# Optimization experiments

Measured on AMD Instinct MI355X. Metric: run time of the kernel, lower is better.

The kernel has to match this reference:

```python
import jax, jax.numpy as jnp
import numpy as np

N_TOKENS = 8192
D_MODEL = 1024
HD_DIM = 4096
N_VEC = 32
N_EXP = 12


def setup_inputs() -> dict:
    key = jax.random.key(0)
    k1, k2, k3, k4, k5 = jax.random.split(key, 5)
    # Glorot-style scaling for the bases so activations stay O(1)
    s_up = (2.0 / (D_MODEL + HD_DIM)) ** 0.5
    return {
        "inputs": jax.random.normal(k1, (N_TOKENS, D_MODEL), dtype=jnp.float32),
        "shared_basis_up": jax.random.normal(k2, (N_VEC, D_MODEL, HD_DIM), dtype=jnp.float32) * s_up,
        "shared_basis_down": jax.random.normal(k3, (N_VEC, HD_DIM, D_MODEL), dtype=jnp.float32) * s_up,
        "expert_coeffs_up": jax.random.normal(k4, (N_EXP, N_VEC), dtype=jnp.float32) * 0.5,
        "expert_coeffs_down": jax.random.normal(k5, (N_EXP, N_VEC), dtype=jnp.float32) * 0.5,
        "expert_bias": jnp.zeros((N_EXP, D_MODEL), dtype=jnp.float32),
        "expert_idx": 3,
    }


def reference(inputs, shared_basis_up, shared_basis_down, expert_coeffs_up,
              expert_coeffs_down, expert_bias, expert_idx):
    coeffs_up = expert_coeffs_up[expert_idx]      # [v]
    coeffs_down = expert_coeffs_down[expert_idx]  # [v]
    bias = expert_bias[expert_idx]                # [d_model]
    # Reconstruct expert weights from shared basis
    W_up = jnp.einsum('v,vdh->dh', coeffs_up, shared_basis_up)      # [d_model, hd_dim]
    W_down = jnp.einsum('v,vhd->hd', coeffs_down, shared_basis_down)  # [hd_dim, d_model]
    hidden = jax.nn.gelu(inputs @ W_up, approximate=False)  # TF default gelu is exact (erf)
    return hidden @ W_down + bias
```

## Files before the change

kernel.cpp:

```cpp
#include <hip/hip_runtime.h>
#include <cstdint>

#define NTOK 8192
#define DMODEL 1024
#define HDDIM 4096
#define NVEC 32

typedef float f32x4_v __attribute__((ext_vector_type(4)));
typedef __bf16 bf16x8 __attribute__((ext_vector_type(8)));
typedef unsigned short u16x4 __attribute__((ext_vector_type(4)));
typedef unsigned short u16x8 __attribute__((ext_vector_type(8)));

__device__ __forceinline__ unsigned short f2bf(float f) {
  union { float f; uint32_t u; } x; x.f = f;
  uint32_t r = (x.u + 0x7FFFu + ((x.u >> 16) & 1u)) >> 16;
  return (unsigned short)r;
}

__device__ __forceinline__ float gelu_fast(float x) {
  float t = x * x;
  float z = x * (2.3022082f + 0.1029440f * t);
  float e = exp2f(-z);
  return x / (1.0f + e);
}

#define VMCNT(n) asm volatile("s_waitcnt vmcnt(" #n ")" ::: "memory")

__device__ __forceinline__ void gload16(const unsigned short* g, unsigned short* lds)
{
  __builtin_amdgcn_global_load_lds((__attribute__((address_space(1))) void*)g,
                                   (__attribute__((address_space(3))) void*)lds,
                                   16, 0, 0);
}

__device__ __forceinline__
void reconstruct_body(const float* __restrict__ basis,
                      const float* __restrict__ coeffs,
                      int e, unsigned short* __restrict__ outT,
                      int X, int Y, int tile, int stag, char* smem, int t)
{
  float (*lds)[260] = (float (*)[260])smem;
  const int xtiles = X >> 4;
  const int bx = tile % xtiles;
  const int by = tile / xtiles;
  const int x0 = bx << 4, y0 = by << 8;
  const int w  = t >> 6, l = t & 63;

  f32x4_v acc[4];
  #pragma unroll
  for (int i = 0; i < 4; ++i) acc[i] = (f32x4_v){0.f, 0.f, 0.f, 0.f};

  const size_t mat = (size_t)X * (size_t)Y;
  uint32_t roff[4];
  #pragma unroll
  for (int i = 0; i < 4; ++i)
    roff[i] = (uint32_t)(x0 + w * 4 + i) * (uint32_t)Y + (uint32_t)(y0 + l * 4);

  #pragma unroll 4
  for (int vv = 0; vv < NVEC; ++vv) {
    const int v = (vv + stag) & (NVEC - 1);
    const float cv = coeffs[e * NVEC + v];
    const float* pv = basis + (size_t)v * mat;
    #pragma unroll
    for (int i = 0; i < 4; ++i) {
      f32x4_v d = __builtin_nontemporal_load((const f32x4_v*)(pv + roff[i]));
      acc[i] += cv * d;
    }
  }

  #pragma unroll
  for (int i = 0; i < 4; ++i)
    *(f32x4_v*)&lds[w * 4 + i][l * 4] = acc[i];
  __syncthreads();

  const int y = y0 + t;
  u16x8 o0, o1;
  #pragma unroll
  for (int x = 0; x < 8; ++x)  o0[x] = f2bf(lds[x][t]);
  #pragma unroll
  for (int x = 0; x < 8; ++x)  o1[x] = f2bf(lds[8 + x][t]);
  unsigned short* dst = outT + (size_t)y * X + x0;
  *(u16x8*)dst = o0;
  *(u16x8*)(dst + 8) = o1;
}

__global__ __launch_bounds__(256)
void p1_kernel(const float* __restrict__ inputs,
               const float* __restrict__ basis_up,
               const float* __restrict__ cup,
               const int* __restrict__ eidx_p,
               unsigned short* __restrict__ A_bf,
               unsigned short* __restrict__ WupT)
{
  __shared__ __align__(16) char smem[16 * 260 * 4];
  const int bid = blockIdx.x;
  if (bid < 1024) {
    reconstruct_body(basis_up, cup, *eidx_p, WupT, DMODEL, HDDIM, bid, bid,
                     smem, threadIdx.x);
  } else {
    const int n4 = NTOK * DMODEL / 4;
    const int stride = 512 * 256;
    for (int i = (bid - 1024) * 256 + threadIdx.x; i < n4; i += stride) {
      f32x4_v v = ((const f32x4_v*)inputs)[i];
      u16x4 u;
      #pragma unroll
      for (int j = 0; j < 4; ++j) u[j] = f2bf(v[j]);
      ((u16x4*)A_bf)[i] = u;
    }
  }
}

__global__ __launch_bounds__(512)
void p2_kernel(const unsigned short* __restrict__ A,
               const unsigned short* __restrict__ Bt,
               unsigned short* __restrict__ Cbf,
               const float* __restrict__ basis_down,
               const float* __restrict__ cdn,
               const int* __restrict__ eidx_p,
               unsigned short* __restrict__ WdnT)
{
  constexpr int BM = 256, BN = 256, BK = 32, CHM = 8, CHN = 8;
  constexpr int FM = BM / 32, FN = BN / 64;
  constexpr int P = (FM * FN) / 16;
  constexpr int SLOT = (BM + BN) * BK * 2;
  constexpr int L = SLOT / 16 / 512;
  constexpr int LPP = L / P;
  constexpr int ACH = BM * 4;
  constexpr int JA = ACH / 512;

  __shared__ __align__(16) char smem[4 * SLOT];

  const int bid = blockIdx.x;

  if (bid & 1) {
    const int half = threadIdx.x >> 8;
    const int tile = (bid >> 1) * 2 + half;
    reconstruct_body(basis_down, cdn, *eidx_p, WdnT, HDDIM, DMODEL,
                     tile, bid + half, smem + half * 16640, threadIdx.x & 255);
    return;
  }

  const int gtile = bid >> 1;
  const int K = DMODEL, N = HDDIM;
  const int ncn = (N / BN) / CHN;
  const int xcd = gtile & 7;
  const int idx = gtile >> 3;
  const int bm  = (xcd / ncn) * CHM + idx / CHN;
  const int bn  = (xcd % ncn) * CHN + idx % CHN;
  const int m0 = bm * BM, n0 = bn * BN;

  const int tid = threadIdx.x;
  const int w = tid >> 6, l = tid & 63;
  const int wm = w >> 2, wn = w & 3;
  const int lrow = l & 15, lkc = l >> 4;

  uint32_t soff[L];
  #pragma unroll
  for (int j = 0; j < L; ++j) {
    const int q = tid + j * 512;
    if (j < JA) {
      const int r = q >> 2, cs = (q & 3) ^ ((r >> 1) & 3);
      soff[j] = (uint32_t)(m0 + r) * (uint32_t)K + cs * 8;
    } else {
      const int q2 = q - ACH;
      const int r = q2 >> 2, cs = (q2 & 3) ^ ((r >> 1) & 3);
      soff[j] = (uint32_t)(n0 + r) * (uint32_t)K + cs * 8;
    }
  }

  int aoff[FM], boff[FN];
  #pragma unroll
  for (int f = 0; f < FM; ++f) {
    const int r = wm * (BM / 2) + f * 16 + lrow;
    aoff[f] = r * 64 + ((lkc ^ ((r >> 1) & 3)) << 4);
  }
  #pragma unroll
  for (int n_ = 0; n_ < FN; ++n_) {
    const int r = wn * (BN / 4) + n_ * 16 + lrow;
    boff[n_] = BM * 64 + r * 64 + ((lkc ^ ((r >> 1) & 3)) << 4);
  }

  f32x4_v acc[FM][FN];
  #pragma unroll
  for (int f = 0; f < FM; ++f)
    #pragma unroll
    for (int n_ = 0; n_ < FN; ++n_) acc[f][n_] = (f32x4_v){0.f, 0.f, 0.f, 0.f};

  const int NT = K / BK;

  for (int tt = 0; tt < 3; ++tt) {
    char* sb = smem + tt * SLOT;
    #pragma unroll
    for (int j = 0; j < L; ++j)
      gload16((j < JA ? A : Bt) + soff[j] + tt * BK,
              (unsigned short*)(sb + (tid + j * 512) * 16));
  }
  VMCNT(8);
  __builtin_amdgcn_s_barrier();
  __builtin_amdgcn_sched_barrier(0);

  bf16x8 bfr[FN];
  for (int t = 0; t < NT; ++t) {
    const char* sb = smem + (t & 3) * SLOT;
    char* pb = smem + ((t + 3) & 3) * SLOT;
    const bool do_stage = (t + 3 < NT);
    #pragma unroll
    for (int p = 0; p < P; ++p) {
      bf16x8 af[4];
      #pragma unroll
      for (int m_ = 0; m_ < 4; ++m_)
        af[m_] = *(const bf16x8*)(sb + aoff[p * 4 + m_]);
      if (p == 0) {
        #pragma unroll
        for (int n_ = 0; n_ < FN; ++n_)
          bfr[n_] = *(const bf16x8*)(sb + boff[n_]);
      }
      if (do_stage) {
        #pragma unroll
        for (int jj = 0; jj < LPP; ++jj) {
          const int j = p * LPP + jj;
          gload16((j < JA ? A : Bt) + soff[j] + (t + 3) * BK,
                  (unsigned short*)(pb + (tid + j * 512) * 16));
        }
      }
      __builtin_amdgcn_s_barrier();
      __builtin_amdgcn_s_setprio(1);
      #pragma unroll
      for (int m_ = 0; m_ < 4; ++m_)
        #pragma unroll
        for (int n_ = 0; n_ < FN; ++n_)
          acc[p * 4 + m_][n_] = __builtin_amdgcn_mfma_f32_16x16x32_bf16(
              af[m_], bfr[n_], acc[p * 4 + m_][n_], 0, 0, 0);
      __builtin_amdgcn_s_setprio(0);
      if (p == P - 1) {
        if (t < NT - 3)       { VMCNT(8); }
        else if (t == NT - 3) { VMCNT(4); }
        else if (t == NT - 2) { VMCNT(0); }
      }
      __builtin_amdgcn_s_barrier();
      __builtin_amdgcn_sched_barrier(0);
    }
  }

  const int colq = l & 15;
  const int rowq = (l >> 4) * 4;
  #pragma unroll
  for (int f = 0; f < FM; ++f)
    #pragma unroll
    for (int n_ = 0; n_ < FN; ++n_) {
      const int col = n0 + wn * (BN / 4) + n_ * 16 + colq;
      #pragma unroll
      for (int r = 0; r < 4; ++r) {
        const int row = m0 + wm * (BM / 2) + f * 16 + rowq + r;
        Cbf[(size_t)row * N + col] = f2bf(gelu_fast(acc[f][n_][r]));
      }
    }
}

template<int CHM, int CHN>
__global__ __launch_bounds__(512)
void gemm_k64(const unsigned short* __restrict__ A,
              const unsigned short* __restrict__ Bt,
              float* __restrict__ Cf,
              const float* __restrict__ bias,
              const int* __restrict__ eidx_p,
              int M, int N, int K)
{
  constexpr int BM = 128, BN = 256, BK = 64;
  constexpr int SLOT = (BM + BN) * BK * 2;
  constexpr int L = 6, JA = 2;
  __shared__ __align__(16) char smem[3 * SLOT];

  const int nb  = N / BN;
  const int ncn = nb / CHN;
  const int xcd = blockIdx.x & 7;
  const int idx = blockIdx.x >> 3;
  const int bm  = (xcd / ncn) * CHM + idx / CHN;
  const int bn  = (xcd % ncn) * CHN + idx % CHN;
  const int m0 = bm * BM, n0 = bn * BN;

  const int tid = threadIdx.x;
  const int w = tid >> 6, l = tid & 63;
  const int wm = w >> 2, wn = w & 3;
  const int lrow = l & 15, lkc = l >> 4;

  uint32_t soff[L];
  #pragma unroll
  for (int j = 0; j < L; ++j) {
    const int q = tid + j * 512;
    if (j < JA) {
      const int r = q >> 3, cs = (q & 7) ^ (r & 7);
      soff[j] = (uint32_t)(m0 + r) * (uint32_t)K + cs * 8;
    } else {
      const int q2 = q - 1024;
      const int r = q2 >> 3, cs = (q2 & 7) ^ (r & 7);
      soff[j] = (uint32_t)(n0 + r) * (uint32_t)K + cs * 8;
    }
  }

  int abase[4], aswz[4], bbase[4], bswz[4];
  #pragma unroll
  for (int f = 0; f < 4; ++f) {
    const int r = wm * 64 + f * 16 + lrow;
    abase[f] = r * 128; aswz[f] = r & 7;
  }
  #pragma unroll
  for (int n_ = 0; n_ < 4; ++n_) {
    const int r = wn * 64 + n_ * 16 + lrow;
    bbase[n_] = 16384 + r * 128; bswz[n_] = r & 7;
  }

  f32x4_v acc[4][4];
  #pragma unroll
  for (int f = 0; f < 4; ++f)
    #pragma unroll
    for (int n_ = 0; n_ < 4; ++n_) acc[f][n_] = (f32x4_v){0.f, 0.f, 0.f, 0.f};

  const int NT = K / BK;

  for (int tt = 0; tt < 2; ++tt) {
    char* sb = smem + tt * SLOT;
    #pragma unroll
    for (int j = 0; j < L; ++j)
      gload16((j < JA ? A : Bt) + soff[j] + tt * BK,
              (unsigned short*)(sb + (tid + j * 512) * 16));
  }
  VMCNT(6);
  __builtin_amdgcn_s_barrier();
  __builtin_amdgcn_sched_barrier(0);

  int cur = 0, pf = 2;
  for (int t = 0; t < NT; ++t) {
    const char* sb = smem + cur * SLOT;
    char* pb = smem + pf * SLOT;
    const bool do_stage = (t + 2 < NT);
    #pragma unroll
    for (int p = 0; p < 2; ++p) {
      bf16x8 af[4], bfr[4];
      #pragma unroll
      for (int m_ = 0; m_ < 4; ++m_)
        af[m_] = *(const bf16x8*)(sb + abase[m_] + ((((p << 2) + lkc) ^ aswz[m_]) << 4));
      #pragma unroll
      for (int n_ = 0; n_ < 4; ++n_)
        bfr[n_] = *(const bf16x8*)(sb + bbase[n_] + ((((p << 2) + lkc) ^ bswz[n_]) << 4));
      if (do_stage) {
        #pragma unroll
        for (int jj = 0; jj < 3; ++jj) {
          const int j = p * 3 + jj;
          gload16((j < JA ? A : Bt) + soff[j] + (t + 2) * BK,
                  (unsigned short*)(pb + (tid + j * 512) * 16));
        }
      }
      __builtin_amdgcn_s_barrier();
      __builtin_amdgcn_s_setprio(1);
      #pragma unroll
      for (int m_ = 0; m_ < 4; ++m_)
        #pragma unroll
        for (int n_ = 0; n_ < 4; ++n_)
          acc[m_][n_] = __builtin_amdgcn_mfma_f32_16x16x32_bf16(
              af[m_], bfr[n_], acc[m_][n_], 0, 0, 0);
      __builtin_amdgcn_s_setprio(0);
      if (p == 1) {
        if (t < NT - 2)       { VMCNT(6); }
        else if (t == NT - 2) { VMCNT(0); }
      }
      __builtin_amdgcn_s_barrier();
      __builtin_amdgcn_sched_barrier(0);
    }
    cur = (cur == 2) ? 0 : cur + 1;
    pf  = (pf == 2) ? 0 : pf + 1;
  }

  const int colq = l & 15;
  const int rowq = (l >> 4) * 4;
  const int e = *eidx_p;
  const float* brow = bias + (size_t)e * N;
  #pragma unroll
  for (int n_ = 0; n_ < 4; ++n_) {
    const int col = n0 + wn * 64 + n_ * 16 + colq;
    const float bv = brow[col];
    #pragma unroll
    for (int f = 0; f < 4; ++f)
      #pragma unroll
      for (int r = 0; r < 4; ++r) {
        const int row = m0 + wm * 64 + f * 16 + rowq + r;
        Cf[(size_t)row * N + col] = acc[f][n_][r] + bv;
      }
  }
}

extern "C" void kernel_launch(void* const* d_in, const int* in_sizes, int n_in,
                              void* d_out, int out_size, void* d_ws, size_t ws_size,
                              hipStream_t stream)
{
  const float* inputs     = (const float*)d_in[0];
  const float* basis_up   = (const float*)d_in[1];
  const float* basis_down = (const float*)d_in[2];
  const float* cup        = (const float*)d_in[3];
  const float* cdn        = (const float*)d_in[4];
  const float* bias       = (const float*)d_in[5];
  const int*   eidx       = (const int*)d_in[6];
  float*       out        = (float*)d_out;

  char* ws = (char*)d_ws;
  unsigned short* A_bf   = (unsigned short*)(ws);
  unsigned short* hidden = (unsigned short*)(ws + (16u << 20));
  unsigned short* WupT   = (unsigned short*)(ws + (80u << 20));
  unsigned short* WdnT   = (unsigned short*)(ws + (88u << 20));

  p1_kernel<<<1536, 256, 0, stream>>>(
      inputs, basis_up, cup, eidx, A_bf, WupT);

  p2_kernel<<<1024, 512, 0, stream>>>(
      A_bf, WupT, hidden, basis_down, cdn, eidx, WdnT);

  gemm_k64<8, 4><<<256, 512, 0, stream>>>(
      hidden, WdnT, out, bias, eidx, NTOK, DMODEL, HDDIM);
}
```

Before: 318.2 us.

## Retile down-projection GEMM to 256x256 tiles with 4-stage BK=32 pipeline

Replaces the second GEMM's 128x256 tile (BK=64, 3-slot buffer) with a 256x256 tile using BK=32 and a 4-slot, 3-deep prefetch ring, with a new swizzle for 64-byte rows. Each wave now holds 8x4 accumulator fragments and reuses its B fragments across two A half-passes, which raises arithmetic intensity per LDS read. The grid drops from 256 to 128 blocks. On a 256-CU part that leaves half the CUs idle and roughly doubles register pressure, traded against fewer global and LDS loads per FLOP.

After: 360.9 us. +13.4%, slower.

```diff
diff --git a/kernel.cpp b/kernel.cpp
--- a/kernel.cpp
+++ b/kernel.cpp
@@ -257,22 +257,25 @@
     }
 }
 
-template<int CHM, int CHN>
 __global__ __launch_bounds__(512)
-void gemm_k64(const unsigned short* __restrict__ A,
-              const unsigned short* __restrict__ Bt,
-              float* __restrict__ Cf,
-              const float* __restrict__ bias,
-              const int* __restrict__ eidx_p,
-              int M, int N, int K)
-{
-  constexpr int BM = 128, BN = 256, BK = 64;
+void g2_kernel(const unsigned short* __restrict__ A,
+               const unsigned short* __restrict__ Bt,
+               float* __restrict__ Cf,
+               const float* __restrict__ bias,
+               const int* __restrict__ eidx_p)
+{
+  constexpr int BM = 256, BN = 256, BK = 32, CHM = 8, CHN = 2;
+  constexpr int FM = 8, FN = 4;
+  constexpr int P = 2;
   constexpr int SLOT = (BM + BN) * BK * 2;
-  constexpr int L = 6, JA = 2;
-  __shared__ __align__(16) char smem[3 * SLOT];
-
-  const int nb  = N / BN;
-  const int ncn = nb / CHN;
+  constexpr int L = 4, LPP = 2;
+  constexpr int ACH = BM * 4;
+  constexpr int JA = 2;
+  const int K = HDDIM, N = DMODEL;
+
+  __shared__ __align__(16) char smem[4 * SLOT];
+
+  const int ncn = (N / BN) / CHN;
   const int xcd = blockIdx.x & 7;
   const int idx = blockIdx.x >> 3;
   const int bm  = (xcd / ncn) * CHM + idx / CHN;
@@ -289,65 +292,67 @@
   for (int j = 0; j < L; ++j) {
     const int q = tid + j * 512;
     if (j < JA) {
-      const int r = q >> 3, cs = (q & 7) ^ (r & 7);
+      const int r = q >> 2, cs = (q & 3) ^ ((r >> 1) & 3);
       soff[j] = (uint32_t)(m0 + r) * (uint32_t)K + cs * 8;
     } else {
-      const int q2 = q - 1024;
-      const int r = q2 >> 3, cs = (q2 & 7) ^ (r & 7);
+      const int q2 = q - ACH;
+      const int r = q2 >> 2, cs = (q2 & 3) ^ ((r >> 1) & 3);
       soff[j] = (uint32_t)(n0 + r) * (uint32_t)K + cs * 8;
     }
   }
 
-  int abase[4], aswz[4], bbase[4], bswz[4];
-  #pragma unroll
-  for (int f = 0; f < 4; ++f) {
-    const int r = wm * 64 + f * 16 + lrow;
-    abase[f] = r * 128; aswz[f] = r & 7;
-  }
-  #pragma unroll
-  for (int n_ = 0; n_ < 4; ++n_) {
-    const int r = wn * 64 + n_ * 16 + lrow;
-    bbase[n_] = 16384 + r * 128; bswz[n_] = r & 7;
-  }
-
-  f32x4_v acc[4][4];
-  #pragma unroll
-  for (int f = 0; f < 4; ++f)
-    #pragma unroll
-    for (int n_ = 0; n_ < 4; ++n_) acc[f][n_] = (f32x4_v){0.f, 0.f, 0.f, 0.f};
+  int aoff[FM], boff[FN];
+  #pragma unroll
+  for (int f = 0; f < FM; ++f) {
+    const int r = wm * (BM / 2) + f * 16 + lrow;
+    aoff[f] = r * 64 + ((lkc ^ ((r >> 1) & 3)) << 4);
+  }
+  #pragma unroll
+  for (int n_ = 0; n_ < FN; ++n_) {
+    const int r = wn * (BN / 4) + n_ * 16 + lrow;
+    boff[n_] = BM * 64 + r * 64 + ((lkc ^ ((r >> 1) & 3)) << 4);
+  }
+
+  f32x4_v acc[FM][FN];
+  #pragma unroll
+  for (int f = 0; f < FM; ++f)
+    #pragma unroll
+    for (int n_ = 0; n_ < FN; ++n_) acc[f][n_] = (f32x4_v){0.f, 0.f, 0.f, 0.f};
 
   const int NT = K / BK;
 
-  for (int tt = 0; tt < 2; ++tt) {
+  for (int tt = 0; tt < 3; ++tt) {
     char* sb = smem + tt * SLOT;
     #pragma unroll
     for (int j = 0; j < L; ++j)
       gload16((j < JA ? A : Bt) + soff[j] + tt * BK,
               (unsigned short*)(sb + (tid + j * 512) * 16));
   }
-  VMCNT(6);
+  VMCNT(8);
   __builtin_amdgcn_s_barrier();
   __builtin_amdgcn_sched_barrier(0);
 
-  int cur = 0, pf = 2;
+  bf16x8 bfr[FN];
   for (int t = 0; t < NT; ++t) {
-    const char* sb = smem + cur * SLOT;
-    char* pb = smem + pf * SLOT;
-    const bool do_stage = (t + 2 < NT);
-    #pragma unroll
-    for (int p = 0; p < 2; ++p) {
-      bf16x8 af[4], bfr[4];
+    const char* sb = smem + (t & 3) * SLOT;
+    char* pb = smem + ((t + 3) & 3) * SLOT;
+    const bool do_stage = (t + 3 < NT);
+    #pragma unroll
+    for (int p = 0; p < P; ++p) {
+      bf16x8 af[4];
       #pragma unroll
       for (int m_ = 0; m_ < 4; ++m_)
-        af[m_] = *(const bf16x8*)(sb + abase[m_] + ((((p << 2) + lkc) ^ aswz[m_]) << 4));
-      #pragma unroll
-      for (int n_ = 0; n_ < 4; ++n_)
-        bfr[n_] = *(const bf16x8*)(sb + bbase[n_] + ((((p << 2) + lkc) ^ bswz[n_]) << 4));
+        af[m_] = *(const bf16x8*)(sb + aoff[p * 4 + m_]);
+      if (p == 0) {
+        #pragma unroll
+        for (int n_ = 0; n_ < FN; ++n_)
+          bfr[n_] = *(const bf16x8*)(sb + boff[n_]);
+      }
       if (do_stage) {
         #pragma unroll
-        for (int jj = 0; jj < 3; ++jj) {
-          const int j = p * 3 + jj;
-          gload16((j < JA ? A : Bt) + soff[j] + (t + 2) * BK,
+        for (int jj = 0; jj < LPP; ++jj) {
+          const int j = p * LPP + jj;
+          gload16((j < JA ? A : Bt) + soff[j] + (t + 3) * BK,
                   (unsigned short*)(pb + (tid + j * 512) * 16));
         }
       }
@@ -356,19 +361,18 @@
       #pragma unroll
       for (int m_ = 0; m_ < 4; ++m_)
         #pragma unroll
-        for (int n_ = 0; n_ < 4; ++n_)
-          acc[m_][n_] = __builtin_amdgcn_mfma_f32_16x16x32_bf16(
-              af[m_], bfr[n_], acc[m_][n_], 0, 0, 0);
+        for (int n_ = 0; n_ < FN; ++n_)
+          acc[p * 4 + m_][n_] = __builtin_amdgcn_mfma_f32_16x16x32_bf16(
+              af[m_], bfr[n_], acc[p * 4 + m_][n_], 0, 0, 0);
       __builtin_amdgcn_s_setprio(0);
-      if (p == 1) {
-        if (t < NT - 2)       { VMCNT(6); }
+      if (p == P - 1) {
+        if (t < NT - 3)       { VMCNT(8); }
+        else if (t == NT - 3) { VMCNT(4); }
         else if (t == NT - 2) { VMCNT(0); }
       }
       __builtin_amdgcn_s_barrier();
       __builtin_amdgcn_sched_barrier(0);
     }
-    cur = (cur == 2) ? 0 : cur + 1;
-    pf  = (pf == 2) ? 0 : pf + 1;
   }
 
   const int colq = l & 15;
@@ -376,14 +380,14 @@
   const int e = *eidx_p;
   const float* brow = bias + (size_t)e * N;
   #pragma unroll
-  for (int n_ = 0; n_ < 4; ++n_) {
-    const int col = n0 + wn * 64 + n_ * 16 + colq;
+  for (int n_ = 0; n_ < FN; ++n_) {
+    const int col = n0 + wn * (BN / 4) + n_ * 16 + colq;
     const float bv = brow[col];
     #pragma unroll
-    for (int f = 0; f < 4; ++f)
+    for (int f = 0; f < FM; ++f)
       #pragma unroll
       for (int r = 0; r < 4; ++r) {
-        const int row = m0 + wm * 64 + f * 16 + rowq + r;
+        const int row = m0 + wm * (BM / 2) + f * 16 + rowq + r;
         Cf[(size_t)row * N + col] = acc[f][n_][r] + bv;
       }
   }
@@ -414,6 +418,6 @@
   p2_kernel<<<1024, 512, 0, stream>>>(
       A_bf, WupT, hidden, basis_down, cdn, eidx, WdnT);
 
-  gemm_k64<8, 4><<<256, 512, 0, stream>>>(
-      hidden, WdnT, out, bias, eidx, NTOK, DMODEL, HDDIM);
-}
+  g2_kernel<<<128, 512, 0, stream>>>(
+      hidden, WdnT, out, bias, eidx);
+}
```
